# Optimization experiments

Measured on AMD Instinct MI355X. Metric: run time of the kernel, lower is better.

Reference implementation:

```python
import jax, jax.numpy as jnp
import numpy as np

B, N, S, C_IN = 8, 1024, 64, 1
H = 32  # hidden_ch


def _mpnn(W, b, x, g):
    # Faithful to MPNN(concat_h=False): messages[b,c,m,n] = x[b,c,m] * g[b,n,m],
    # flattened to (c m) channels and hit by a 1x1 conv W of shape (H, c, m).
    # out[b,u,n] = sum_{c,m} W[u,c,m] * x[b,c,m] * g[b,n,m] + b[u]
    t = jnp.einsum('ucm,bcm->bum', W, x)          # tiny contraction over c
    return jnp.einsum('bum,bnm->bun', t, g) + b[None, :, None]


def setup_inputs() -> dict:
    key = jax.random.key(0)
    ks = jax.random.split(key, 14)
    gate_scale = 1.0 / np.sqrt(C_IN * N)

    def gate_w(k):
        return jax.random.normal(k, (H, C_IN, N), jnp.float32) * gate_scale

    return {
        'x': jax.random.normal(ks[0], (B, N, S, C_IN), jnp.float32),
        'mask': jnp.ones((B, N, S, C_IN), dtype=bool),  # unused by the module
        'fwd_graph': jax.random.uniform(ks[1], (B, N, N), jnp.float32),
        # GRU gate MPNN 1x1-conv weights, reshaped (H, C_IN*N, 1) -> (H, C_IN, N)
        'Wf': gate_w(ks[2]), 'bf': jnp.zeros((H,), jnp.float32),
        'Wu': gate_w(ks[3]), 'bu': jnp.zeros((H,), jnp.float32),
        'Wc': gate_w(ks[4]), 'bc': jnp.zeros((H,), jnp.float32),
        'h0': jnp.zeros((H, N), jnp.float32),
        'W1': jax.random.normal(ks[5], (H, H), jnp.float32) / np.sqrt(H),
        'b1': jnp.zeros((H,), jnp.float32),
        'W2': jax.random.normal(ks[6], (H, 2 * H), jnp.float32) / np.sqrt(2 * H),
        'b2': jnp.zeros((H,), jnp.float32),
        # LocalConv1D: per-node 1x1 conv, weights (n, out_ch, 2H), bias (n, out_ch)
        'Wd': jax.random.normal(ks[7], (N, C_IN, 2 * H), jnp.float32) / np.sqrt(2 * H),
        'bd': jnp.zeros((N, C_IN), jnp.float32),
    }


def reference(x, mask, fwd_graph, Wf, bf, Wu, bu, Wc, bc, h0, W1, b1, W2, b2, Wd, bd):
    del mask  # present in the torch signature but never used
    b = x.shape[0]
    xs = jnp.transpose(x, (2, 0, 3, 1))  # (s, b, c, n)
    g = fwd_graph
    h_init = jnp.broadcast_to(h0[None], (b, H, N))

    def step(h, x_t):
        # NOTE: with concat_h=False the forget gate r = sigmoid(MPNN_f(x)) only
        # rescales h passed into c_gate, which ignores h entirely -> r (Wf, bf)
        # has no effect on the output; omitted here (same math).
        u = jax.nn.sigmoid(_mpnn(Wu, bu, x_t, g))
        c = jnp.tanh(_mpnn(Wc, bc, x_t, g))
        h_new = u * h + (1.0 - u) * c
        return h_new, None

    h, _ = jax.lax.scan(step, h_init, xs)

    # Prediction head (only the last step's prediction is returned: pred[:, :, -1:])
    x1 = jax.nn.leaky_relu(jnp.einsum('uh,bhn->bun', W1, h) + b1[None, :, None])
    x2 = jax.nn.leaky_relu(
        jnp.einsum('uk,bkn->bun', W2, jnp.concatenate([x1, h], axis=1)) + b2[None, :, None])
    dec_in = jnp.concatenate([x2, h], axis=1)  # (b, 2H, n)
    # LocalConv1D (per-node weights), fully batched:
    x_hat = jnp.einsum('nok,bkn->bon', Wd, dec_in) + bd.T[None, :, :]  # (b, c, n)
    return jnp.transpose(x_hat, (0, 2, 1))[:, :, None, :]  # (b, n, 1, c)
```

## Files before the change

kernel.cpp:

```cpp
#include <hip/hip_runtime.h>
#include <hip/hip_bf16.h>
#include <hip/hip_fp16.h>

#define Bsz 8
#define Nn 1024
#define Ss 64
#define Hh 32

typedef _Float16 half8 __attribute__((ext_vector_type(8)));
typedef _Float16 half4 __attribute__((ext_vector_type(4)));
typedef float f32x4 __attribute__((ext_vector_type(4)));

__device__ __forceinline__ void gload_lds16(const _Float16* g, _Float16* l) {
  __builtin_amdgcn_global_load_lds(
      (const __attribute__((address_space(1))) unsigned int*)g,
      (__attribute__((address_space(3))) unsigned int*)l, 16, 0, 0);
}

__global__ __launch_bounds__(256)
void build_a(const float* __restrict__ x, const float* __restrict__ Wu,
             const float* __restrict__ Wc, _Float16* __restrict__ Ah) {
  const int b = blockIdx.x >> 6;
  const int t = blockIdx.x & 63;
  const int tid = threadIdx.x;
  __shared__ float xs[Nn];
  for (int m = tid; m < Nn; m += 256) xs[m] = x[((size_t)(b * Nn + m)) * Ss + t];
  __syncthreads();
  const int m4 = tid * 4;
  const float4 xv = *(const float4*)(&xs[m4]);
  const size_t bbase = (size_t)b * 4096;
#pragma unroll 4
  for (int i = 0; i < 64; ++i) {
    const int u = i & 31;
    const int gate = i >> 5;
    const float* W = (gate == 0) ? (Wu + (size_t)u * Nn) : (Wc + (size_t)u * Nn);
    const float4 w = *(const float4*)(&W[m4]);
    half4 o;
    o[0] = (_Float16)(w.x * xv.x);
    o[1] = (_Float16)(w.y * xv.y);
    o[2] = (_Float16)(w.z * xv.z);
    o[3] = (_Float16)(w.w * xv.w);
    const size_t row = bbase + (size_t)u * 128 + gate * 64 + t;
    *(half4*)(&Ah[row * Nn + m4]) = o;
  }
}

__global__ __launch_bounds__(256)
void conv_g(const float* __restrict__ g, _Float16* __restrict__ gh) {
  const size_t i = ((size_t)blockIdx.x * 256 + threadIdx.x) * 4;
  const float4 v = *(const float4*)(&g[i]);
  half4 o;
  o[0] = (_Float16)v.x; o[1] = (_Float16)v.y; o[2] = (_Float16)v.z; o[3] = (_Float16)v.w;
  *(half4*)(&gh[i]) = o;
}

#define CP 130
__global__ __launch_bounds__(256)
void gemm_recur(const _Float16* __restrict__ A, const _Float16* __restrict__ G,
                const float* __restrict__ bu, const float* __restrict__ bc,
                const float* __restrict__ h0, float* __restrict__ H) {
  __shared__ __align__(16) char smem[128 * CP * 2];
  _Float16* As = (_Float16*)smem;
  _Float16* Gs = (_Float16*)(smem + 8192);
  _Float16* Cs = (_Float16*)smem;

  const int u = blockIdx.x;
  const int col0 = blockIdx.y * 128;
  const int b = blockIdx.z;
  const int tid = threadIdx.x;
  const int lane = tid & 63;
  const int wave = tid >> 6;
  const int wr = (wave >> 1) * 64;
  const int wc = (wave & 1) * 64;

  const _Float16* Ab = A + ((size_t)b * 4096 + (size_t)u * 128) * 1024;
  const _Float16* Gb = G + ((size_t)b * 1024 + col0) * 1024;

  f32x4 acc[4][4] = {};

  const int srow = lane >> 2;
  const int scol = (lane & 3) * 8;

  for (int kk = 0; kk < 32; ++kk) {
    const int k0 = kk * 32;
#pragma unroll
    for (int i = 0; i < 2; ++i) {
      const int chunk = wave * 2 + i;
      const int r = chunk * 16 + srow;
      gload_lds16(Ab + (size_t)r * 1024 + k0 + scol, As + chunk * 512);
      gload_lds16(Gb + (size_t)r * 1024 + k0 + scol, Gs + chunk * 512);
    }
    __syncthreads();

    half8 af[4], bf[4];
#pragma unroll
    for (int mi = 0; mi < 4; ++mi)
      af[mi] = *(const half8*)(&As[(wr + mi * 16 + (lane & 15)) * 32 + (lane >> 4) * 8]);
#pragma unroll
    for (int ni = 0; ni < 4; ++ni)
      bf[ni] = *(const half8*)(&Gs[(wc + ni * 16 + (lane & 15)) * 32 + (lane >> 4) * 8]);
#pragma unroll
    for (int mi = 0; mi < 4; ++mi)
#pragma unroll
      for (int ni = 0; ni < 4; ++ni)
        acc[mi][ni] = __builtin_amdgcn_mfma_f32_16x16x32_f16(af[mi], bf[ni], acc[mi][ni], 0, 0, 0);
    __syncthreads();
  }

#pragma unroll
  for (int mi = 0; mi < 4; ++mi)
#pragma unroll
    for (int ni = 0; ni < 4; ++ni)
#pragma unroll
      for (int j = 0; j < 4; ++j) {
        const int r = wr + mi * 16 + (lane >> 4) * 4 + j;
        const int c = wc + ni * 16 + (lane & 15);
        Cs[r * CP + c] = (_Float16)acc[mi][ni][j];
      }
  __syncthreads();

  if (tid < 128) {
    const int n = col0 + tid;
    const float bias_u = bu[u];
    const float bias_c = bc[u];
    float h = h0[u * Nn + n];
    for (int t = 0; t < 64; ++t) {
      const float yu = (float)Cs[t * CP + tid] + bias_u;
      const float yc = (float)Cs[(64 + t) * CP + tid] + bias_c;
      const float s = 1.f / (1.f + __expf(-yu));
      const float e = __expf(-2.f * fabsf(yc));
      float th = (1.f - e) / (1.f + e);
      th = yc < 0.f ? -th : th;
      h = s * h + (1.f - s) * th;
    }
    H[((size_t)b * Hh + u) * Nn + n] = h;
  }
}

__global__ __launch_bounds__(256)
void head(const float* __restrict__ H, const float* __restrict__ W1,
          const float* __restrict__ b1, const float* __restrict__ W2,
          const float* __restrict__ b2, const float* __restrict__ Wd,
          const float* __restrict__ bd, float* __restrict__ out) {
  const int b = blockIdx.x >> 2;
  const int n = (blockIdx.x & 3) * 256 + threadIdx.x;
  const float* Hb = H + (size_t)b * Hh * Nn;
  float h[32];
#pragma unroll
  for (int u = 0; u < 32; ++u) h[u] = Hb[u * Nn + n];
  float x1[32];
#pragma unroll 4
  for (int v = 0; v < 32; ++v) {
    float a = b1[v];
#pragma unroll
    for (int u = 0; u < 32; ++u) a += W1[v * 32 + u] * h[u];
    x1[v] = a > 0.f ? a : 0.01f * a;
  }
  float x2[32];
#pragma unroll 4
  for (int v = 0; v < 32; ++v) {
    float a = b2[v];
#pragma unroll
    for (int u = 0; u < 32; ++u) a += W2[v * 64 + u] * x1[u];
#pragma unroll
    for (int u = 0; u < 32; ++u) a += W2[v * 64 + 32 + u] * h[u];
    x2[v] = a > 0.f ? a : 0.01f * a;
  }
  float o = bd[n];
#pragma unroll
  for (int v = 0; v < 32; ++v) o += Wd[n * 64 + v] * x2[v];
#pragma unroll
  for (int v = 0; v < 32; ++v) o += Wd[n * 64 + 32 + v] * h[v];
  out[(size_t)b * Nn + n] = o;
}

extern "C" void kernel_launch(void* const* d_in, const int* in_sizes, int n_in,
                              void* d_out, int out_size, void* d_ws, size_t ws_size,
                              hipStream_t stream) {
  const float* x  = (const float*)d_in[0];
  const float* g  = (const float*)d_in[2];
  const float* Wu = (const float*)d_in[5];
  const float* bu = (const float*)d_in[6];
  const float* Wc = (const float*)d_in[7];
  const float* bc = (const float*)d_in[8];
  const float* h0 = (const float*)d_in[9];
  const float* W1 = (const float*)d_in[10];
  const float* b1 = (const float*)d_in[11];
  const float* W2 = (const float*)d_in[12];
  const float* b2 = (const float*)d_in[13];
  const float* Wd = (const float*)d_in[14];
  const float* bd = (const float*)d_in[15];
  float* out = (float*)d_out;

  char* ws = (char*)d_ws;
  _Float16* Ah = (_Float16*)(ws);
  _Float16* gh = (_Float16*)(ws + (size_t)(64u << 20));
  float*    Hx = (float*)  (ws + (size_t)(80u << 20));

  build_a<<<512, 256, 0, stream>>>(x, Wu, Wc, Ah);
  conv_g<<<8192, 256, 0, stream>>>(g, gh);
  dim3 gg(32, 8, 8);
  gemm_recur<<<gg, 256, 0, stream>>>(Ah, gh, bu, bc, h0, Hx);
  head<<<32, 256, 0, stream>>>(Hx, W1, b1, W2, b2, Wd, bd, out);
}
```

Before: 252.2 us.

## Form W*x operand on the fly in GEMM instead of materializing 64MB A

Drops the build_a kernel, which wrote a 64MB fp16 A matrix (W[u,m]*x[b,t,m] per b,u,t). A small prep kernel now writes transposed fp16 x and fp16 gate weights, and the GEMM multiplies them in registers when it loads each A fragment. This cuts A global traffic roughly by the factor of H and fuses the g conversion into the same launch. It also swizzles the C staging buffer in LDS instead of padding it, and splits the head over more, smaller blocks. The risk is extra fp16 rounding, since the product is now formed from already-rounded fp16 inputs.

```diff
diff --git a/kernel.cpp b/kernel.cpp
--- a/kernel.cpp
+++ b/kernel.cpp
@@ -18,50 +18,68 @@
 }
 
 __global__ __launch_bounds__(256)
-void build_a(const float* __restrict__ x, const float* __restrict__ Wu,
-             const float* __restrict__ Wc, _Float16* __restrict__ Ah) {
-  const int b = blockIdx.x >> 6;
-  const int t = blockIdx.x & 63;
+void prep(const float* __restrict__ x, const float* __restrict__ Wu,
+          const float* __restrict__ Wc, const float* __restrict__ g,
+          _Float16* __restrict__ xT, _Float16* __restrict__ Wh,
+          _Float16* __restrict__ gh) {
   const int tid = threadIdx.x;
-  __shared__ float xs[Nn];
-  for (int m = tid; m < Nn; m += 256) xs[m] = x[((size_t)(b * Nn + m)) * Ss + t];
-  __syncthreads();
-  const int m4 = tid * 4;
-  const float4 xv = *(const float4*)(&xs[m4]);
-  const size_t bbase = (size_t)b * 4096;
-#pragma unroll 4
-  for (int i = 0; i < 64; ++i) {
-    const int u = i & 31;
-    const int gate = i >> 5;
-    const float* W = (gate == 0) ? (Wu + (size_t)u * Nn) : (Wc + (size_t)u * Nn);
-    const float4 w = *(const float4*)(&W[m4]);
+  if (blockIdx.x < 64) {
+    const int b = blockIdx.x >> 3;
+    const int m0 = (blockIdx.x & 7) * 128;
+    __shared__ _Float16 tile[128 * 68];
+    const int m = tid >> 1;
+    const int hf = tid & 1;
+    const float* src = x + ((size_t)(b * Nn + m0 + m)) * Ss + hf * 32;
+#pragma unroll
+    for (int i = 0; i < 8; ++i) {
+      const float4 v = *(const float4*)(src + i * 4);
+      half4 o;
+      o[0] = (_Float16)v.x; o[1] = (_Float16)v.y;
+      o[2] = (_Float16)v.z; o[3] = (_Float16)v.w;
+      *(half4*)(&tile[m * 68 + hf * 32 + i * 4]) = o;
+    }
+    __syncthreads();
+    const int t = tid & 63;
+    const int q = tid >> 6;
+    _Float16* dst = xT + ((size_t)(b * 64 + t)) * Nn + m0 + q * 32;
+#pragma unroll
+    for (int i = 0; i < 4; ++i) {
+      half8 o;
+#pragma unroll
+      for (int e = 0; e < 8; ++e) o[e] = tile[(q * 32 + i * 8 + e) * 68 + t];
+      *(half8*)(dst + i * 8) = o;
+    }
+  } else if (blockIdx.x < 72) {
+    const int w = blockIdx.x - 64;
+    const size_t i0 = ((size_t)(w * 256 + tid)) * 32;
+#pragma unroll
+    for (int i = 0; i < 8; ++i) {
+      const size_t i4 = i0 + i * 4;
+      const float* s = (i4 < 32768) ? (Wu + i4) : (Wc + (i4 - 32768));
+      const float4 v = *(const float4*)s;
+      half4 o;
+      o[0] = (_Float16)v.x; o[1] = (_Float16)v.y;
+      o[2] = (_Float16)v.z; o[3] = (_Float16)v.w;
+      *(half4*)(&Wh[i4]) = o;
+    }
+  } else {
+    const size_t i = ((size_t)(blockIdx.x - 72) * 256 + tid) * 4;
+    const float4 v = *(const float4*)(&g[i]);
     half4 o;
-    o[0] = (_Float16)(w.x * xv.x);
-    o[1] = (_Float16)(w.y * xv.y);
-    o[2] = (_Float16)(w.z * xv.z);
-    o[3] = (_Float16)(w.w * xv.w);
-    const size_t row = bbase + (size_t)u * 128 + gate * 64 + t;
-    *(half4*)(&Ah[row * Nn + m4]) = o;
+    o[0] = (_Float16)v.x; o[1] = (_Float16)v.y;
+    o[2] = (_Float16)v.z; o[3] = (_Float16)v.w;
+    *(half4*)(&gh[i]) = o;
   }
 }
 
 __global__ __launch_bounds__(256)
-void conv_g(const float* __restrict__ g, _Float16* __restrict__ gh) {
-  const size_t i = ((size_t)blockIdx.x * 256 + threadIdx.x) * 4;
-  const float4 v = *(const float4*)(&g[i]);
-  half4 o;
-  o[0] = (_Float16)v.x; o[1] = (_Float16)v.y; o[2] = (_Float16)v.z; o[3] = (_Float16)v.w;
-  *(half4*)(&gh[i]) = o;
-}
-
-#define CP 130
-__global__ __launch_bounds__(256)
-void gemm_recur(const _Float16* __restrict__ A, const _Float16* __restrict__ G,
-                const float* __restrict__ bu, const float* __restrict__ bc,
-                const float* __restrict__ h0, float* __restrict__ H) {
-  __shared__ __align__(16) char smem[128 * CP * 2];
-  _Float16* As = (_Float16*)smem;
-  _Float16* Gs = (_Float16*)(smem + 8192);
+void gemm_recur(const _Float16* __restrict__ xT, const _Float16* __restrict__ Wh,
+                const _Float16* __restrict__ G, const float* __restrict__ bu,
+                const float* __restrict__ bc, const float* __restrict__ h0,
+                float* __restrict__ H) {
+  __shared__ __align__(16) char smem[32768];
+  _Float16* Xs = (_Float16*)smem;
+  _Float16* Gs = (_Float16*)(smem + 4096);
   _Float16* Cs = (_Float16*)smem;
 
   const int u = blockIdx.x;
@@ -72,33 +90,40 @@
   const int wave = tid >> 6;
   const int wr = (wave >> 1) * 64;
   const int wc = (wave & 1) * 64;
-
-  const _Float16* Ab = A + ((size_t)b * 4096 + (size_t)u * 128) * 1024;
-  const _Float16* Gb = G + ((size_t)b * 1024 + col0) * 1024;
+  const int gate = wave >> 1;
+
+  const _Float16* Xb = xT + (size_t)b * 64 * Nn;
+  const _Float16* Gb = G + ((size_t)b * Nn + col0) * Nn;
+  const _Float16* Wg = Wh + ((size_t)gate * 32 + u) * Nn;
 
   f32x4 acc[4][4] = {};
 
   const int srow = lane >> 2;
   const int scol = (lane & 3) * 8;
+  const int koff = (lane >> 4) * 8;
 
   for (int kk = 0; kk < 32; ++kk) {
     const int k0 = kk * 32;
+    gload_lds16(Xb + (size_t)(wave * 16 + srow) * Nn + k0 + scol,
+                Xs + wave * 512);
 #pragma unroll
     for (int i = 0; i < 2; ++i) {
       const int chunk = wave * 2 + i;
-      const int r = chunk * 16 + srow;
-      gload_lds16(Ab + (size_t)r * 1024 + k0 + scol, As + chunk * 512);
-      gload_lds16(Gb + (size_t)r * 1024 + k0 + scol, Gs + chunk * 512);
-    }
+      gload_lds16(Gb + (size_t)(chunk * 16 + srow) * Nn + k0 + scol,
+                  Gs + chunk * 512);
+    }
+    const half8 wv = *(const half8*)(Wg + k0 + koff);
     __syncthreads();
 
     half8 af[4], bf[4];
 #pragma unroll
-    for (int mi = 0; mi < 4; ++mi)
-      af[mi] = *(const half8*)(&As[(wr + mi * 16 + (lane & 15)) * 32 + (lane >> 4) * 8]);
+    for (int mi = 0; mi < 4; ++mi) {
+      const half8 x8 = *(const half8*)(&Xs[(mi * 16 + (lane & 15)) * 32 + koff]);
+      af[mi] = wv * x8;
+    }
 #pragma unroll
     for (int ni = 0; ni < 4; ++ni)
-      bf[ni] = *(const half8*)(&Gs[(wc + ni * 16 + (lane & 15)) * 32 + (lane >> 4) * 8]);
+      bf[ni] = *(const half8*)(&Gs[(wc + ni * 16 + (lane & 15)) * 32 + koff]);
 #pragma unroll
     for (int mi = 0; mi < 4; ++mi)
 #pragma unroll
@@ -115,7 +140,7 @@
       for (int j = 0; j < 4; ++j) {
         const int r = wr + mi * 16 + (lane >> 4) * 4 + j;
         const int c = wc + ni * 16 + (lane & 15);
-        Cs[r * CP + c] = (_Float16)acc[mi][ni][j];
+        Cs[r * 128 + (c ^ (((r >> 2) & 3) << 3))] = (_Float16)acc[mi][ni][j];
       }
   __syncthreads();
 
@@ -125,8 +150,9 @@
     const float bias_c = bc[u];
     float h = h0[u * Nn + n];
     for (int t = 0; t < 64; ++t) {
-      const float yu = (float)Cs[t * CP + tid] + bias_u;
-      const float yc = (float)Cs[(64 + t) * CP + tid] + bias_c;
+      const int cc = tid ^ (((t >> 2) & 3) << 3);
+      const float yu = (float)Cs[t * 128 + cc] + bias_u;
+      const float yc = (float)Cs[(64 + t) * 128 + cc] + bias_c;
       const float s = 1.f / (1.f + __expf(-yu));
       const float e = __expf(-2.f * fabsf(yc));
       float th = (1.f - e) / (1.f + e);
@@ -137,13 +163,13 @@
   }
 }
 
-__global__ __launch_bounds__(256)
+__global__ __launch_bounds__(128)
 void head(const float* __restrict__ H, const float* __restrict__ W1,
           const float* __restrict__ b1, const float* __restrict__ W2,
           const float* __restrict__ b2, const float* __restrict__ Wd,
           const float* __restrict__ bd, float* __restrict__ out) {
-  const int b = blockIdx.x >> 2;
-  const int n = (blockIdx.x & 3) * 256 + threadIdx.x;
+  const int b = blockIdx.x >> 3;
+  const int n = (blockIdx.x & 7) * 128 + threadIdx.x;
   const float* Hb = H + (size_t)b * Hh * Nn;
   float h[32];
 #pragma unroll
@@ -193,13 +219,13 @@
   float* out = (float*)d_out;
 
   char* ws = (char*)d_ws;
-  _Float16* Ah = (_Float16*)(ws);
-  _Float16* gh = (_Float16*)(ws + (size_t)(64u << 20));
-  float*    Hx = (float*)  (ws + (size_t)(80u << 20));
-
-  build_a<<<512, 256, 0, stream>>>(x, Wu, Wc, Ah);
-  conv_g<<<8192, 256, 0, stream>>>(g, gh);
+  _Float16* xT = (_Float16*)(ws);
+  _Float16* Wh = (_Float16*)(ws + (size_t)(1u << 20));
+  _Float16* gh = (_Float16*)(ws + (size_t)(2u << 20));
+  float*    Hx = (float*)  (ws + (size_t)(18u << 20));
+
+  prep<<<72 + 8192, 256, 0, stream>>>(x, Wu, Wc, g, xT, Wh, gh);
   dim3 gg(32, 8, 8);
-  gemm_recur<<<gg, 256, 0, stream>>>(Ah, gh, bu, bc, h0, Hx);
-  head<<<32, 256, 0, stream>>>(Hx, W1, b1, W2, b2, Wd, bd, out);
-}
+  gemm_recur<<<gg, 256, 0, stream>>>(xT, Wh, gh, bu, bc, h0, Hx);
+  head<<<64, 128, 0, stream>>>(Hx, W1, b1, W2, b2, Wd, bd, out);
+}
```

New measurement: 234.9 us. -6.9%, faster.
